# Kernel optimization log

Hardware: AMD Instinct MI355X
Metric: run time of the kernel (lower is better)

Reference implementation:

```python
import jax, jax.numpy as jnp
import numpy as np

B, S, E, H, M, Q = 2, 2048, 768, 12, 768, 4
D = E // H  # head_dim = 64
EPS = 1e-5


def _layernorm(x, g, b):
    m = jnp.mean(x, axis=-1, keepdims=True)
    v = jnp.mean((x - m) ** 2, axis=-1, keepdims=True)
    return (x - m) / jnp.sqrt(v + EPS) * g + b


def setup_inputs() -> dict:
    key = jax.random.key(0)
    ks = jax.random.split(key, 12)
    w = lambda k, shape, s=0.02: (jax.random.normal(k, shape) * s).astype(jnp.float32)
    return {
        "x": jax.random.normal(ks[0], (B, S, E), dtype=jnp.float32),
        "ln1_g": jnp.ones((E,), jnp.float32), "ln1_b": jnp.zeros((E,), jnp.float32),
        "wq": w(ks[1], (E, E)), "bq": jnp.zeros((E,), jnp.float32),
        "wk": w(ks[2], (E, E)), "bk": jnp.zeros((E,), jnp.float32),
        "wv": w(ks[3], (E, E)), "bv": jnp.zeros((E,), jnp.float32),
        "wo": w(ks[4], (E, E)), "bo": jnp.zeros((E,), jnp.float32),
        "ln2_g": jnp.ones((E,), jnp.float32), "ln2_b": jnp.zeros((E,), jnp.float32),
        "w1": w(ks[5], (E, Q * M)), "b1": jnp.zeros((Q * M,), jnp.float32),
        "wvqc": w(ks[6], (M, M)), "bvqc": jnp.zeros((M,), jnp.float32),
        "w2": w(ks[7], (Q * M, E)), "b2": jnp.zeros((E,), jnp.float32),
    }


def reference(x, ln1_g, ln1_b, wq, bq, wk, bk, wv, bv, wo, bo,
              ln2_g, ln2_b, w1, b1, wvqc, bvqc, w2, b2):
    b, s, e = x.shape
    h, d = H, e // H

    # --- attention branch (pre-norm, per-query-L2-normalized logits) ---
    xn = _layernorm(x, ln1_g, ln1_b)
    q = (xn @ wq + bq).reshape(b, s, h, d).transpose(0, 2, 1, 3)  # bhsd
    k = (xn @ wk + bk).reshape(b, s, h, d).transpose(0, 2, 1, 3)
    v = (xn @ wv + bv).reshape(b, s, h, d).transpose(0, 2, 1, 3)

    qk = jnp.einsum('bhsd,bhtd->bhst', q, k)                       # [B,H,S,S]
    q_norm2 = jnp.clip(jnp.sum(q * q, axis=-1, keepdims=True), 1e-5)  # [B,H,S,1]
    logits = qk / jnp.sqrt(d * q_norm2)
    attn = jax.nn.softmax(logits, axis=-1)
    vals = jnp.einsum('bhst,bhtd->bhsd', attn, v)
    vals = vals.transpose(0, 2, 1, 3).reshape(b, s, e)
    x = x + (vals @ wo + bo)  # residual; attn dropout is identity in eval

    # --- quantum-style FeedForward with overlapping q_stride slices ---
    xn2 = _layernorm(x, ln2_g, ln2_b)
    hmid = xn2 @ w1 + b1                                           # [B,S,Q*M]
    m = wvqc.shape[0]
    qstride = w1.shape[1] // m
    # overlapping slices h[..., i:i+M] for i in 0..Q-1, stacked on a new axis
    sl = jnp.stack([hmid[..., i:i + m] for i in range(qstride)], axis=2)  # [B,S,Q,M]
    hv = sl @ wvqc + bvqc                                          # vqc linear
    hv = hv.transpose(0, 1, 3, 2).reshape(b, s, qstride * m)       # interleave
    hv = jax.nn.gelu(hv, approximate=False)
    out = x + (hv @ w2 + b2)
    return out
```

## Files before the change

kernel.cpp:

```cpp
#include <hip/hip_runtime.h>
#include <hip/hip_bf16.h>
#include <math.h>

typedef unsigned short ushort_t;
typedef __attribute__((ext_vector_type(4))) short s16x4;
typedef __attribute__((ext_vector_type(8))) short short8;
typedef __attribute__((ext_vector_type(8))) __bf16 bf16x8;
typedef __attribute__((ext_vector_type(4))) float f32x4;
typedef __attribute__((ext_vector_type(4))) unsigned u32x4;

#define SDIM 2048
#define EDIM 768
#define NTOK 4096

static __device__ __forceinline__ ushort_t f2bf(float f) {
  unsigned u = __builtin_bit_cast(unsigned, f);
  u += 0x7fff + ((u >> 16) & 1);
  return (ushort_t)(u >> 16);
}
static __device__ __forceinline__ float bf2f(ushort_t h) {
  return __builtin_bit_cast(float, (unsigned)h << 16);
}
static __device__ __forceinline__ f32x4 mfma16(short8 a, short8 b, f32x4 c) {
  return __builtin_amdgcn_mfma_f32_16x16x32_bf16(
      __builtin_bit_cast(bf16x8, a), __builtin_bit_cast(bf16x8, b), c, 0, 0, 0);
}
static __device__ __forceinline__ void gload_lds16(const void* g, void* l) {
  __builtin_amdgcn_global_load_lds(
      (const __attribute__((address_space(1))) void*)g,
      (__attribute__((address_space(3))) void*)l, 16, 0, 0);
}
static __device__ __forceinline__ unsigned cvtpk(float lo, float hi) {
  unsigned r;
  asm("v_cvt_pk_bf16_f32 %0, %1, %2" : "=v"(r) : "v"(lo), "v"(hi));
  return r;
}
static __device__ __forceinline__ float exp2fast(float x) {
  float r;
  asm("v_exp_f32 %0, %1" : "=v"(r) : "v"(x));
  return r;
}

__global__ void k_pre(const float* __restrict__ wq, const float* __restrict__ wk,
                      const float* __restrict__ wv, const float* __restrict__ wo,
                      const float* __restrict__ wvqc, const float* __restrict__ w2,
                      const float* __restrict__ w1, const float* __restrict__ x,
                      const float* __restrict__ ln1g, const float* __restrict__ ln1b,
                      ushort_t* __restrict__ oqkv, ushort_t* __restrict__ owo,
                      ushort_t* __restrict__ ovqc, ushort_t* __restrict__ w2T,
                      ushort_t* __restrict__ w1s, ushort_t* __restrict__ xn) {
  const int y = blockIdx.y;
  const int tx = threadIdx.x, ty = threadIdx.y;
  __shared__ float tile[32][33];
  __shared__ float red[8];
  if (y < 216) {
    const float* in;
    ushort_t* out;
    int R, r0;
    const int c0 = blockIdx.x * 32;
    if (y < 120) {
      const int z = y / 24, ry = y - z * 24;
      in = z == 0 ? wq : z == 1 ? wk : z == 2 ? wv : z == 3 ? wo : wvqc;
      out = z < 3 ? oqkv + (size_t)z * 768 * 768 : (z == 3 ? owo : ovqc);
      R = 768;
      r0 = ry * 32;
    } else {
      in = w2;
      out = w2T;
      R = 3072;
      r0 = (y - 120) * 32;
    }
#pragma unroll
    for (int i = 0; i < 32; i += 8)
      tile[ty + i][tx] = in[(size_t)(r0 + ty + i) * 768 + c0 + tx];
    __syncthreads();
#pragma unroll
    for (int i = 0; i < 32; i += 8)
      out[(size_t)(c0 + ty + i) * R + r0 + tx] = f2bf(tile[tx][ty + i]);
  } else if (y < 312) {
    const int idx = ((y - 216) * 24 + blockIdx.x) * 256 + ty * 32 + tx;
    const int e = idx / 768, m = idx - (idx / 768) * 768;
#pragma unroll
    for (int i = 0; i < 4; i++)
      w1s[((size_t)i * 768 + e) * 768 + m] = f2bf(w1[(size_t)e * 3072 + i + m]);
  } else {
    const int row = (y - 312) * 24 + blockIdx.x;
    if (row >= NTOK) return;
    const int t = ty * 32 + tx;
    const float* xr = x + (size_t)row * EDIM;
    float v0 = xr[t], v1 = xr[t + 256], v2 = xr[t + 512];
    float s = v0 + v1 + v2;
    float s2 = v0 * v0 + v1 * v1 + v2 * v2;
#pragma unroll
    for (int m = 32; m; m >>= 1) {
      s += __shfl_xor(s, m);
      s2 += __shfl_xor(s2, m);
    }
    const int wid = t >> 6, lane = t & 63;
    if (lane == 0) { red[wid] = s; red[4 + wid] = s2; }
    __syncthreads();
    s = red[0] + red[1] + red[2] + red[3];
    s2 = red[4] + red[5] + red[6] + red[7];
    float mean = s * (1.f / EDIM);
    float var = s2 * (1.f / EDIM) - mean * mean;
    float rstd = rsqrtf(var + 1e-5f);
    ushort_t* orow = xn + (size_t)row * EDIM;
    orow[t] = f2bf((v0 - mean) * rstd * ln1g[t] + ln1b[t]);
    orow[t + 256] = f2bf((v1 - mean) * rstd * ln1g[t + 256] + ln1b[t + 256]);
    orow[t + 512] = f2bf((v2 - mean) * rstd * ln1g[t + 512] + ln1b[t + 512]);
  }
}

__global__ void k_vT(const ushort_t* __restrict__ in, ushort_t* __restrict__ out) {
  __shared__ ushort_t tile[32][34];
  int bh = blockIdx.z;
  int t0 = blockIdx.x * 32, d0 = blockIdx.y * 32;
  const ushort_t* ib = in + (size_t)bh * SDIM * 64;
  ushort_t* ob = out + (size_t)bh * 64 * SDIM;
  int tx = threadIdx.x, ty = threadIdx.y;
#pragma unroll
  for (int i = 0; i < 32; i += 8)
    tile[ty + i][tx] = ib[(size_t)(t0 + ty + i) * 64 + d0 + tx];
  __syncthreads();
  const int T = t0 + tx, tb = T & ~63, tl = T & 63;
  const int tperm =
      tb + 32 * (tl >> 5) + 8 * ((tl >> 2) & 3) + 4 * ((tl >> 4) & 1) + (tl & 3);
#pragma unroll
  for (int i = 0; i < 32; i += 8)
    ob[(size_t)(d0 + ty + i) * SDIM + tperm] = tile[tx][ty + i];
}

__global__ __launch_bounds__(256) void k_b1eff(const float* __restrict__ b1,
                                               const ushort_t* __restrict__ wvqcT,
                                               const float* __restrict__ bvqc,
                                               float* __restrict__ b1e) {
  const int n = blockIdx.x;
  const int i = n & 3, j = n >> 2;
  const int t = threadIdx.x;
  float s = 0.f;
  for (int m = t; m < 768; m += 256)
    s += b1[i + m] * bf2f(wvqcT[(size_t)j * 768 + m]);
#pragma unroll
  for (int mm = 32; mm; mm >>= 1) s += __shfl_xor(s, mm);
  __shared__ float red[4];
  if ((t & 63) == 0) red[t >> 6] = s;
  __syncthreads();
  if (t == 0) b1e[n] = red[0] + red[1] + red[2] + red[3] + bvqc[j];
}

__global__ __launch_bounds__(256) void k_ln(const float* __restrict__ x,
                                            const float* __restrict__ gam,
                                            const float* __restrict__ bet,
                                            ushort_t* __restrict__ out) {
  const int row = blockIdx.x, t = threadIdx.x;
  const float* xr = x + (size_t)row * EDIM;
  float v0 = xr[t], v1 = xr[t + 256], v2 = xr[t + 512];
  float s = v0 + v1 + v2;
  float s2 = v0 * v0 + v1 * v1 + v2 * v2;
#pragma unroll
  for (int m = 32; m; m >>= 1) { s += __shfl_xor(s, m); s2 += __shfl_xor(s2, m); }
  __shared__ float red[8];
  const int wid = t >> 6, lane = t & 63;
  if (lane == 0) { red[wid] = s; red[4 + wid] = s2; }
  __syncthreads();
  s = red[0] + red[1] + red[2] + red[3];
  s2 = red[4] + red[5] + red[6] + red[7];
  float mean = s * (1.f / EDIM);
  float var = s2 * (1.f / EDIM) - mean * mean;
  float rstd = rsqrtf(var + 1e-5f);
  ushort_t* orow = out + (size_t)row * EDIM;
  orow[t] = f2bf((v0 - mean) * rstd * gam[t] + bet[t]);
  orow[t + 256] = f2bf((v1 - mean) * rstd * gam[t + 256] + bet[t + 256]);
  orow[t + 512] = f2bf((v2 - mean) * rstd * gam[t + 512] + bet[t + 512]);
}

template <int MODE, int BM, int BN, int BK>
__global__ __launch_bounds__(256) void k_gemm(
    const ushort_t* __restrict__ A, const ushort_t* __restrict__ Bt, int lda,
    int ldb, int kc, const float* __restrict__ b0, const float* __restrict__ b1p,
    const float* __restrict__ b2p, float* __restrict__ outF,
    const float* __restrict__ resid, ushort_t* __restrict__ o0,
    ushort_t* __restrict__ o1, ushort_t* __restrict__ o2, int ldc) {
  constexpr int MT = BM / 32, NT = BN / 32;
  constexpr int KCH = BK / 8;
  constexpr int NPA = BM * BK / 2048;
  constexpr int NPB = BN * BK / 2048;
  constexpr int ROWSP = 2048 / BK;
  constexpr int KK = BK / 32;
  __shared__ ushort_t As[2][BM * BK];
  __shared__ ushort_t Bs[2][BN * BK];
  const int t = threadIdx.x;
  const int m0 = blockIdx.x * BM, n0 = blockIdx.y * BN;
  if (MODE == 3) Bt += (size_t)blockIdx.z * 768 * 768;
  const int koff = (MODE == 5) ? blockIdx.z * kc : 0;
  const int srow = t / KCH, sch = t % KCH;
  const int xs = (BK == 64) ? (srow & 7) : ((srow >> 1) & 3);
  const int gseg = (sch ^ xs) * 8;
  const ushort_t* ga = A + (size_t)(m0 + srow) * lda + koff + gseg;
  const ushort_t* gb = Bt + (size_t)(n0 + srow) * ldb + koff + gseg;
  const int ldst = t * 8;
  const int lane = t & 63, wid = t >> 6;
  const int g = lane >> 4, c = lane & 15;
  const int wm = (wid >> 1) * (BM / 2), wn = (wid & 1) * (BN / 2);
  const int xc = (BK == 64) ? (c & 7) : ((c >> 1) & 3);
  f32x4 acc[MT][NT] = {};

#define STAGE(BUF, K0)                                                           \
  {                                                                              \
    _Pragma("unroll") for (int p = 0; p < NPA; p++)                              \
        gload_lds16(ga + (K0) + (size_t)(p * ROWSP) * lda,                       \
                    As[BUF] + p * 2048 + ldst);                                  \
    _Pragma("unroll") for (int p = 0; p < NPB; p++)                              \
        gload_lds16(gb + (K0) + (size_t)(p * ROWSP) * ldb,                       \
                    Bs[BUF] + p * 2048 + ldst);                                  \
  }

  STAGE(0, 0);
  __syncthreads();
  int cur = 0;
  for (int k0 = 0; k0 < kc; k0 += BK) {
    if (k0 + BK < kc) STAGE(cur ^ 1, k0 + BK);
    short8 af[KK][MT], bfr[KK][NT];
#pragma unroll
    for (int kk = 0; kk < KK; kk++) {
#pragma unroll
      for (int mt = 0; mt < MT; mt++)
        af[kk][mt] = *(const short8*)(As[cur] + (wm + mt * 16 + c) * BK +
                                      (((g + kk * 4) ^ xc) * 8));
#pragma unroll
      for (int nt = 0; nt < NT; nt++)
        bfr[kk][nt] = *(const short8*)(Bs[cur] + (wn + nt * 16 + c) * BK +
                                       (((g + kk * 4) ^ xc) * 8));
    }
    __builtin_amdgcn_s_setprio(1);
#pragma unroll
    for (int kk = 0; kk < KK; kk++)
#pragma unroll
      for (int mt = 0; mt < MT; mt++)
#pragma unroll
        for (int nt = 0; nt < NT; nt++)
          acc[mt][nt] = mfma16(af[kk][mt], bfr[kk][nt], acc[mt][nt]);
    __builtin_amdgcn_s_setprio(0);
    __syncthreads();
    cur ^= 1;
  }
#undef STAGE

#pragma unroll
  for (int mt = 0; mt < MT; mt++) {
#pragma unroll
    for (int nt = 0; nt < NT; nt++) {
#pragma unroll
      for (int r = 0; r < 4; r++) {
        int row = m0 + wm + mt * 16 + g * 4 + r;
        int col = n0 + wn + nt * 16 + c;
        float val = acc[mt][nt][r];
        if constexpr (MODE == 0) {
          int which = col / 768;
          int nn = col - which * 768;
          int h = nn >> 6, d = nn & 63;
          int bb = row >> 11, s = row & 2047;
          const float* bp = which == 0 ? b0 : (which == 1 ? b1p : b2p);
          ushort_t* dp = which == 0 ? o0 : (which == 1 ? o1 : o2);
          dp[(((size_t)(bb * 12 + h)) * SDIM + s) * 64 + d] = f2bf(val + bp[nn]);
        } else if constexpr (MODE == 1) {
          size_t o = (size_t)row * ldc + col;
          outF[o] = resid[o] + val + b0[col];
        } else if constexpr (MODE == 2) {
          float xg = val + b0[col];
          float z2 = xg * (1.5957691216f + 0.0713548162f * xg * xg);
          float ge = xg / (1.f + __expf(-z2));
          o0[(size_t)row * ldc + col] = f2bf(ge);
        } else if constexpr (MODE == 5) {
          o0[(size_t)blockIdx.z * (NTOK * 768) + (size_t)row * ldc + col] =
              f2bf(val);
        } else {
          o0[((size_t)row * 4 + blockIdx.z) * ldc + col] = f2bf(val);
        }
      }
    }
  }
}

__global__ __launch_bounds__(256) void k_attn(
    const ushort_t* __restrict__ q, const ushort_t* __restrict__ k,
    const ushort_t* __restrict__ vt, ushort_t* __restrict__ o0p,
    ushort_t* __restrict__ o1p, float* __restrict__ lpart) {
  const int tid = threadIdx.x;
  const int wid = tid >> 6, lane = tid & 63;
  const int g = lane >> 4, c = lane & 15;
  const int bh = blockIdx.y;
  const int z = blockIdx.z;
  const int tbase = z * (SDIM / 2);
  const int q0 = blockIdx.x * 128 + wid * 32;
  const int bb = bh / 12, h = bh - bb * 12;
  const ushort_t* qb = q + (size_t)bh * SDIM * 64;
  const ushort_t* kb = k + (size_t)bh * SDIM * 64;
  const ushort_t* vb = vt + (size_t)bh * 64 * SDIM;

  __shared__ ushort_t Ks[2][64 * 64];
  __shared__ ushort_t Vs[2][64 * 64];

  short8 bq[2][2];
#pragma unroll
  for (int qg = 0; qg < 2; qg++) {
    short8 a0 = *(const short8*)(qb + (size_t)(q0 + qg * 16 + c) * 64 + g * 8);
    short8 a1 =
        *(const short8*)(qb + (size_t)(q0 + qg * 16 + c) * 64 + 32 + g * 8);
    float s = 0.f;
#pragma unroll
    for (int j = 0; j < 8; j++) {
      float f0 = bf2f((ushort_t)a0[j]), f1 = bf2f((ushort_t)a1[j]);
      s += f0 * f0 + f1 * f1;
    }
    s += __shfl_xor(s, 16);
    s += __shfl_xor(s, 32);
    const float scq = rsqrtf(64.f * fmaxf(s, 1e-5f)) * 1.44269504089f;
#pragma unroll
    for (int j = 0; j < 8; j++) {
      bq[qg][0][j] = (short)f2bf(bf2f((ushort_t)a0[j]) * scq);
      bq[qg][1][j] = (short)f2bf(bf2f((ushort_t)a1[j]) * scq);
    }
  }
  const short8 ones = {0x3F80, 0x3F80, 0x3F80, 0x3F80,
                       0x3F80, 0x3F80, 0x3F80, 0x3F80};

  const int srow = tid >> 3, sj = tid & 7;

#define STAGE(BUF, T0)                                                          \
  {                                                                             \
    _Pragma("unroll") for (int n = 0; n < 2; n++) {                             \
      const int row = n * 32 + srow;                                            \
      const int scol = (sj ^ (row & 7)) * 8;                                    \
      gload_lds16(kb + (size_t)((T0) + row) * 64 + scol,                        \
                  Ks[BUF] + n * 2048 + tid * 8);                                \
      gload_lds16(vb + (size_t)row * SDIM + (T0) + scol,                        \
                  Vs[BUF] + n * 2048 + tid * 8);                                \
    }                                                                           \
  }

  f32x4 accO[2][4] = {};
  f32x4 accL[2] = {};
  const int sw = (c & 7) << 4;

  STAGE(0, tbase);
  __syncthreads();
  int cur = 0;
  for (int tt = 0; tt < SDIM / 128; tt++) {
    const int t0 = tbase + tt * 64;
    if (tt + 1 < SDIM / 128) STAGE(cur ^ 1, t0 + 64);
    const char* Kc = (const char*)Ks[cur];
    const char* Vc = (const char*)Vs[cur];
    f32x4 s0[4] = {}, s1[4] = {};
    __builtin_amdgcn_s_setprio(1);
#pragma unroll
    for (int i = 0; i < 4; i++) {
      const int rb = (i * 16 + c) * 128;
      short8 ka0 = *(const short8*)(Kc + rb + ((g * 16) ^ sw));
      short8 ka1 = *(const short8*)(Kc + rb + ((64 + g * 16) ^ sw));
      s0[i] = mfma16(ka0, bq[0][0], s0[i]);
      s1[i] = mfma16(ka0, bq[1][0], s1[i]);
      s0[i] = mfma16(ka1, bq[0][1], s0[i]);
      s1[i] = mfma16(ka1, bq[1][1], s1[i]);
    }
    __builtin_amdgcn_s_setprio(0);
    u32x4 w00 = {cvtpk(exp2fast(s0[0][0]), exp2fast(s0[0][1])),
                 cvtpk(exp2fast(s0[0][2]), exp2fast(s0[0][3])),
                 cvtpk(exp2fast(s0[1][0]), exp2fast(s0[1][1])),
                 cvtpk(exp2fast(s0[1][2]), exp2fast(s0[1][3]))};
    u32x4 w10 = {cvtpk(exp2fast(s1[0][0]), exp2fast(s1[0][1])),
                 cvtpk(exp2fast(s1[0][2]), exp2fast(s1[0][3])),
                 cvtpk(exp2fast(s1[1][0]), exp2fast(s1[1][1])),
                 cvtpk(exp2fast(s1[1][2]), exp2fast(s1[1][3]))};
    u32x4 w01 = {cvtpk(exp2fast(s0[2][0]), exp2fast(s0[2][1])),
                 cvtpk(exp2fast(s0[2][2]), exp2fast(s0[2][3])),
                 cvtpk(exp2fast(s0[3][0]), exp2fast(s0[3][1])),
                 cvtpk(exp2fast(s0[3][2]), exp2fast(s0[3][3]))};
    u32x4 w11 = {cvtpk(exp2fast(s1[2][0]), exp2fast(s1[2][1])),
                 cvtpk(exp2fast(s1[2][2]), exp2fast(s1[2][3])),
                 cvtpk(exp2fast(s1[3][0]), exp2fast(s1[3][1])),
                 cvtpk(exp2fast(s1[3][2]), exp2fast(s1[3][3]))};
    short8 pa00 = __builtin_bit_cast(short8, w00);
    short8 pa01 = __builtin_bit_cast(short8, w01);
    short8 pa10 = __builtin_bit_cast(short8, w10);
    short8 pa11 = __builtin_bit_cast(short8, w11);
    __builtin_amdgcn_s_setprio(1);
    accL[0] = mfma16(pa00, ones, accL[0]);
    accL[1] = mfma16(pa10, ones, accL[1]);
    accL[0] = mfma16(pa01, ones, accL[0]);
    accL[1] = mfma16(pa11, ones, accL[1]);
#pragma unroll
    for (int dt = 0; dt < 4; dt++) {
      const int vbse = (dt * 16 + c) * 128;
      short8 v0 = *(const short8*)(Vc + vbse + ((g * 16) ^ sw));
      short8 v1 = *(const short8*)(Vc + vbse + ((64 + g * 16) ^ sw));
      accO[0][dt] = mfma16(pa00, v0, accO[0][dt]);
      accO[1][dt] = mfma16(pa10, v0, accO[1][dt]);
      accO[0][dt] = mfma16(pa01, v1, accO[0][dt]);
      accO[1][dt] = mfma16(pa11, v1, accO[1][dt]);
    }
    __builtin_amdgcn_s_setprio(0);
    __syncthreads();
    cur ^= 1;
  }
#undef STAGE

  ushort_t* op = z ? o1p : o0p;
#pragma unroll
  for (int qg = 0; qg < 2; qg++) {
    if (c == 0) {
#pragma unroll
      for (int r = 0; r < 4; r++)
        lpart[((size_t)z * 24 + bh) * SDIM + q0 + qg * 16 + 4 * g + r] =
            accL[qg][r];
    }
#pragma unroll
    for (int dt = 0; dt < 4; dt++)
#pragma unroll
      for (int r = 0; r < 4; r++) {
        int s = q0 + qg * 16 + 4 * g + r;
        op[((size_t)(bb * SDIM + s)) * EDIM + h * 64 + dt * 16 + c] =
            f2bf(accO[qg][dt][r]);
      }
  }
}

__global__ __launch_bounds__(256) void k_comb(const ushort_t* __restrict__ o0p,
                                              const ushort_t* __restrict__ o1p,
                                              const float* __restrict__ lpart,
                                              ushort_t* __restrict__ vals) {
  const int gid = blockIdx.x * 256 + threadIdx.x;
  const int tok = gid / 96, ch = gid - tok * 96;
  const int h = ch >> 3;
  const int bb = tok >> 11, s = tok & 2047;
  const size_t lrow = (size_t)(bb * 12 + h) * SDIM + s;
  const float inv = 1.f / (lpart[lrow] + lpart[(size_t)24 * SDIM + lrow]);
  short8 a = *(const short8*)(o0p + (size_t)gid * 8);
  short8 b = *(const short8*)(o1p + (size_t)gid * 8);
  short8 o;
#pragma unroll
  for (int j = 0; j < 8; j++)
    o[j] = (short)f2bf((bf2f((ushort_t)a[j]) + bf2f((ushort_t)b[j])) * inv);
  *(short8*)(vals + (size_t)gid * 8) = o;
}

__global__ __launch_bounds__(256) void k_fin(const float* __restrict__ x2,
                                             const float* __restrict__ b2,
                                             const ushort_t* __restrict__ p,
                                             float* __restrict__ out) {
  const int i = blockIdx.x * 256 + threadIdx.x;
  f32x4 r = ((const f32x4*)x2)[i];
  f32x4 b = ((const f32x4*)b2)[i % 192];
  s16x4 a0 = ((const s16x4*)p)[i];
  s16x4 a1 = ((const s16x4*)(p + (size_t)NTOK * 768))[i];
  f32x4 o;
#pragma unroll
  for (int j = 0; j < 4; j++)
    o[j] = r[j] + b[j] + bf2f((ushort_t)a0[j]) + bf2f((ushort_t)a1[j]);
  ((f32x4*)out)[i] = o;
}

extern "C" void kernel_launch(void* const* d_in, const int* in_sizes, int n_in,
                              void* d_out, int out_size, void* d_ws, size_t ws_size,
                              hipStream_t stream) {
  const float* x = (const float*)d_in[0];
  const float* ln1g = (const float*)d_in[1];
  const float* ln1b = (const float*)d_in[2];
  const float* wq = (const float*)d_in[3];
  const float* bq = (const float*)d_in[4];
  const float* wk = (const float*)d_in[5];
  const float* bk = (const float*)d_in[6];
  const float* wv = (const float*)d_in[7];
  const float* bv = (const float*)d_in[8];
  const float* wo = (const float*)d_in[9];
  const float* bo = (const float*)d_in[10];
  const float* ln2g = (const float*)d_in[11];
  const float* ln2b = (const float*)d_in[12];
  const float* w1 = (const float*)d_in[13];
  const float* b1 = (const float*)d_in[14];
  const float* wvqc = (const float*)d_in[15];
  const float* bvqc = (const float*)d_in[16];
  const float* w2 = (const float*)d_in[17];
  const float* b2 = (const float*)d_in[18];
  float* out = (float*)d_out;

  char* w = (char*)d_ws;
  ushort_t* xn = (ushort_t*)(w + 0);
  ushort_t* vtb = (ushort_t*)(w + 0);
  ushort_t* xn2 = (ushort_t*)(w + 6291456);
  ushort_t* opart1 = (ushort_t*)(w + 6291456);
  float* x2 = (float*)(w + 12582912);
  ushort_t* qb = (ushort_t*)(w + 25165824);
  ushort_t* kb = (ushort_t*)(w + 31457280);
  ushort_t* vb = (ushort_t*)(w + 37748736);
  ushort_t* vals = (ushort_t*)(w + 44040192);
  ushort_t* G = (ushort_t*)(w + 25165824);
  ushort_t* wqkvT = (ushort_t*)(w + 50528256);
  ushort_t* woT = (ushort_t*)(w + 54067200);
  ushort_t* wvqcT = (ushort_t*)(w + 55246848);
  ushort_t* w1s = (ushort_t*)(w + 56426496);
  float* lpart = (float*)(w + 56426496);
  ushort_t* W1eT = (ushort_t*)(w + 61145088);
  float* b1e = (float*)(w + 65863680);
  ushort_t* w2T = (ushort_t*)(w + 65875968);
  ushort_t* mp = (ushort_t*)(w + 0);

  dim3 tb(32, 8);
  k_pre<<<dim3(24, 483), tb, 0, stream>>>(wq, wk, wv, wo, wvqc, w2, w1, x, ln1g,
                                          ln1b, wqkvT, woT, wvqcT, w2T, w1s, xn);
  k_b1eff<<<3072, 256, 0, stream>>>(b1, wvqcT, bvqc, b1e);
  k_gemm<3, 64, 64, 64><<<dim3(12, 12, 4), 256, 0, stream>>>(
      wvqcT, w1s, 768, 768, 768, nullptr, nullptr, nullptr, nullptr, nullptr,
      W1eT, nullptr, nullptr, 768);
  k_gemm<0, 128, 64, 64><<<dim3(32, 36), 256, 0, stream>>>(
      xn, wqkvT, 768, 768, 768, bq, bk, bv, nullptr, nullptr, qb, kb, vb, 0);
  k_vT<<<dim3(64, 2, 24), tb, 0, stream>>>(vb, vtb);
  k_attn<<<dim3(16, 24, 2), 256, 0, stream>>>(qb, kb, vtb, vals, opart1, lpart);
  k_comb<<<1536, 256, 0, stream>>>(vals, opart1, lpart, vals);
  k_gemm<1, 64, 64, 64><<<dim3(64, 12), 256, 0, stream>>>(
      vals, woT, 768, 768, 768, bo, nullptr, nullptr, x2, x, nullptr, nullptr,
      nullptr, 768);
  k_ln<<<4096, 256, 0, stream>>>(x2, ln2g, ln2b, xn2);
  k_gemm<2, 128, 64, 64><<<dim3(32, 48), 256, 0, stream>>>(
      xn2, W1eT, 768, 768, 768, b1e, nullptr, nullptr, nullptr, nullptr, G,
      nullptr, nullptr, 3072);
  k_gemm<5, 64, 64, 64><<<dim3(64, 12, 2), 256, 0, stream>>>(
      G, w2T, 3072, 3072, 1536, nullptr, nullptr, nullptr, nullptr, nullptr, mp,
      nullptr, nullptr, 768);
  k_fin<<<3072, 256, 0, stream>>>(x2, b2, mp, out);
}
```

Before: 192.8 us.

## Fold bias precompute into prep kernel, widen attention tiles, drop split-K FFN2

The separate b1-effective kernel becomes an extra block row of the prep kernel, computed serially per thread from fp32 wvqc. The attention kernel now gives each wave 64 queries instead of 32, which halves the grid and reuses each K/V LDS tile across more queries. The final FFN GEMM drops split-K plus the separate finish kernel and uses the fused bias+residual epilogue (mode 1) over the full K=3072. This removes launches and an intermediate round trip. In exchange it raises register pressure in attention, lowers grid parallelism, and makes the folded bias loop slow and serial.

New measurement: 232.7 us. +20.7%, slower.

```diff
diff --git a/kernel.cpp b/kernel.cpp
--- a/kernel.cpp
+++ b/kernel.cpp
@@ -3,7 +3,6 @@
 #include <math.h>
 
 typedef unsigned short ushort_t;
-typedef __attribute__((ext_vector_type(4))) short s16x4;
 typedef __attribute__((ext_vector_type(8))) short short8;
 typedef __attribute__((ext_vector_type(8))) __bf16 bf16x8;
 typedef __attribute__((ext_vector_type(4))) float f32x4;
@@ -46,9 +45,11 @@
                       const float* __restrict__ wvqc, const float* __restrict__ w2,
                       const float* __restrict__ w1, const float* __restrict__ x,
                       const float* __restrict__ ln1g, const float* __restrict__ ln1b,
+                      const float* __restrict__ b1, const float* __restrict__ bvqc,
                       ushort_t* __restrict__ oqkv, ushort_t* __restrict__ owo,
                       ushort_t* __restrict__ ovqc, ushort_t* __restrict__ w2T,
-                      ushort_t* __restrict__ w1s, ushort_t* __restrict__ xn) {
+                      ushort_t* __restrict__ w1s, ushort_t* __restrict__ xn,
+                      float* __restrict__ b1e) {
   const int y = blockIdx.y;
   const int tx = threadIdx.x, ty = threadIdx.y;
   __shared__ float tile[32][33];
@@ -83,7 +84,7 @@
 #pragma unroll
     for (int i = 0; i < 4; i++)
       w1s[((size_t)i * 768 + e) * 768 + m] = f2bf(w1[(size_t)e * 3072 + i + m]);
-  } else {
+  } else if (y < 483) {
     const int row = (y - 312) * 24 + blockIdx.x;
     if (row >= NTOK) return;
     const int t = ty * 32 + tx;
@@ -108,6 +109,13 @@
     orow[t] = f2bf((v0 - mean) * rstd * ln1g[t] + ln1b[t]);
     orow[t + 256] = f2bf((v1 - mean) * rstd * ln1g[t + 256] + ln1b[t + 256]);
     orow[t + 512] = f2bf((v2 - mean) * rstd * ln1g[t + 512] + ln1b[t + 512]);
+  } else {
+    const int n = blockIdx.x * 256 + ty * 32 + tx;
+    if (n >= 3072) return;
+    const int i = n & 3, j = n >> 2;
+    float s = 0.f;
+    for (int m = 0; m < 768; m++) s += b1[i + m] * wvqc[(size_t)m * 768 + j];
+    b1e[n] = s + bvqc[j];
   }
 }
 
@@ -128,24 +136,6 @@
 #pragma unroll
   for (int i = 0; i < 32; i += 8)
     ob[(size_t)(d0 + ty + i) * SDIM + tperm] = tile[tx][ty + i];
-}
-
-__global__ __launch_bounds__(256) void k_b1eff(const float* __restrict__ b1,
-                                               const ushort_t* __restrict__ wvqcT,
-                                               const float* __restrict__ bvqc,
-                                               float* __restrict__ b1e) {
-  const int n = blockIdx.x;
-  const int i = n & 3, j = n >> 2;
-  const int t = threadIdx.x;
-  float s = 0.f;
-  for (int m = t; m < 768; m += 256)
-    s += b1[i + m] * bf2f(wvqcT[(size_t)j * 768 + m]);
-#pragma unroll
-  for (int mm = 32; mm; mm >>= 1) s += __shfl_xor(s, mm);
-  __shared__ float red[4];
-  if ((t & 63) == 0) red[t >> 6] = s;
-  __syncthreads();
-  if (t == 0) b1e[n] = red[0] + red[1] + red[2] + red[3] + bvqc[j];
 }
 
 __global__ __launch_bounds__(256) void k_ln(const float* __restrict__ x,
@@ -192,12 +182,11 @@
   const int t = threadIdx.x;
   const int m0 = blockIdx.x * BM, n0 = blockIdx.y * BN;
   if (MODE == 3) Bt += (size_t)blockIdx.z * 768 * 768;
-  const int koff = (MODE == 5) ? blockIdx.z * kc : 0;
   const int srow = t / KCH, sch = t % KCH;
   const int xs = (BK == 64) ? (srow & 7) : ((srow >> 1) & 3);
   const int gseg = (sch ^ xs) * 8;
-  const ushort_t* ga = A + (size_t)(m0 + srow) * lda + koff + gseg;
-  const ushort_t* gb = Bt + (size_t)(n0 + srow) * ldb + koff + gseg;
+  const ushort_t* ga = A + (size_t)(m0 + srow) * lda + gseg;
+  const ushort_t* gb = Bt + (size_t)(n0 + srow) * ldb + gseg;
   const int ldst = t * 8;
   const int lane = t & 63, wid = t >> 6;
   const int g = lane >> 4, c = lane & 15;
@@ -271,9 +260,6 @@
           float z2 = xg * (1.5957691216f + 0.0713548162f * xg * xg);
           float ge = xg / (1.f + __expf(-z2));
           o0[(size_t)row * ldc + col] = f2bf(ge);
-        } else if constexpr (MODE == 5) {
-          o0[(size_t)blockIdx.z * (NTOK * 768) + (size_t)row * ldc + col] =
-              f2bf(val);
         } else {
           o0[((size_t)row * 4 + blockIdx.z) * ldc + col] = f2bf(val);
         }
@@ -292,7 +278,7 @@
   const int bh = blockIdx.y;
   const int z = blockIdx.z;
   const int tbase = z * (SDIM / 2);
-  const int q0 = blockIdx.x * 128 + wid * 32;
+  const int q0 = blockIdx.x * 256 + wid * 64;
   const int bb = bh / 12, h = bh - bb * 12;
   const ushort_t* qb = q + (size_t)bh * SDIM * 64;
   const ushort_t* kb = k + (size_t)bh * SDIM * 64;
@@ -301,9 +287,9 @@
   __shared__ ushort_t Ks[2][64 * 64];
   __shared__ ushort_t Vs[2][64 * 64];
 
-  short8 bq[2][2];
-#pragma unroll
-  for (int qg = 0; qg < 2; qg++) {
+  short8 bq[4][2];
+#pragma unroll
+  for (int qg = 0; qg < 4; qg++) {
     short8 a0 = *(const short8*)(qb + (size_t)(q0 + qg * 16 + c) * 64 + g * 8);
     short8 a1 =
         *(const short8*)(qb + (size_t)(q0 + qg * 16 + c) * 64 + 32 + g * 8);
@@ -339,8 +325,8 @@
     }                                                                           \
   }
 
-  f32x4 accO[2][4] = {};
-  f32x4 accL[2] = {};
+  f32x4 accO[4][4] = {};
+  f32x4 accL[4] = {};
   const int sw = (c & 7) << 4;
 
   STAGE(0, tbase);
@@ -351,55 +337,60 @@
     if (tt + 1 < SDIM / 128) STAGE(cur ^ 1, t0 + 64);
     const char* Kc = (const char*)Ks[cur];
     const char* Vc = (const char*)Vs[cur];
-    f32x4 s0[4] = {}, s1[4] = {};
+    f32x4 s[4][4] = {};
     __builtin_amdgcn_s_setprio(1);
 #pragma unroll
     for (int i = 0; i < 4; i++) {
       const int rb = (i * 16 + c) * 128;
       short8 ka0 = *(const short8*)(Kc + rb + ((g * 16) ^ sw));
       short8 ka1 = *(const short8*)(Kc + rb + ((64 + g * 16) ^ sw));
-      s0[i] = mfma16(ka0, bq[0][0], s0[i]);
-      s1[i] = mfma16(ka0, bq[1][0], s1[i]);
-      s0[i] = mfma16(ka1, bq[0][1], s0[i]);
-      s1[i] = mfma16(ka1, bq[1][1], s1[i]);
+#pragma unroll
+      for (int qg = 0; qg < 4; qg++) {
+        s[qg][i] = mfma16(ka0, bq[qg][0], s[qg][i]);
+        s[qg][i] = mfma16(ka1, bq[qg][1], s[qg][i]);
+      }
     }
     __builtin_amdgcn_s_setprio(0);
-    u32x4 w00 = {cvtpk(exp2fast(s0[0][0]), exp2fast(s0[0][1])),
-                 cvtpk(exp2fast(s0[0][2]), exp2fast(s0[0][3])),
-                 cvtpk(exp2fast(s0[1][0]), exp2fast(s0[1][1])),
-                 cvtpk(exp2fast(s0[1][2]), exp2fast(s0[1][3]))};
-    u32x4 w10 = {cvtpk(exp2fast(s1[0][0]), exp2fast(s1[0][1])),
-                 cvtpk(exp2fast(s1[0][2]), exp2fast(s1[0][3])),
-                 cvtpk(exp2fast(s1[1][0]), exp2fast(s1[1][1])),
-                 cvtpk(exp2fast(s1[1][2]), exp2fast(s1[1][3]))};
-    u32x4 w01 = {cvtpk(exp2fast(s0[2][0]), exp2fast(s0[2][1])),
-                 cvtpk(exp2fast(s0[2][2]), exp2fast(s0[2][3])),
-                 cvtpk(exp2fast(s0[3][0]), exp2fast(s0[3][1])),
-                 cvtpk(exp2fast(s0[3][2]), exp2fast(s0[3][3]))};
-    u32x4 w11 = {cvtpk(exp2fast(s1[2][0]), exp2fast(s1[2][1])),
-                 cvtpk(exp2fast(s1[2][2]), exp2fast(s1[2][3])),
-                 cvtpk(exp2fast(s1[3][0]), exp2fast(s1[3][1])),
-                 cvtpk(exp2fast(s1[3][2]), exp2fast(s1[3][3]))};
-    short8 pa00 = __builtin_bit_cast(short8, w00);
-    short8 pa01 = __builtin_bit_cast(short8, w01);
-    short8 pa10 = __builtin_bit_cast(short8, w10);
-    short8 pa11 = __builtin_bit_cast(short8, w11);
-    __builtin_amdgcn_s_setprio(1);
-    accL[0] = mfma16(pa00, ones, accL[0]);
-    accL[1] = mfma16(pa10, ones, accL[1]);
-    accL[0] = mfma16(pa01, ones, accL[0]);
-    accL[1] = mfma16(pa11, ones, accL[1]);
-#pragma unroll
-    for (int dt = 0; dt < 4; dt++) {
-      const int vbse = (dt * 16 + c) * 128;
-      short8 v0 = *(const short8*)(Vc + vbse + ((g * 16) ^ sw));
-      short8 v1 = *(const short8*)(Vc + vbse + ((64 + g * 16) ^ sw));
-      accO[0][dt] = mfma16(pa00, v0, accO[0][dt]);
-      accO[1][dt] = mfma16(pa10, v0, accO[1][dt]);
-      accO[0][dt] = mfma16(pa01, v1, accO[0][dt]);
-      accO[1][dt] = mfma16(pa11, v1, accO[1][dt]);
-    }
-    __builtin_amdgcn_s_setprio(0);
+#pragma unroll
+    for (int pr = 0; pr < 2; pr++) {
+      const int ca = pr * 2, cbx = pr * 2 + 1;
+      u32x4 wa0 = {cvtpk(exp2fast(s[ca][0][0]), exp2fast(s[ca][0][1])),
+                   cvtpk(exp2fast(s[ca][0][2]), exp2fast(s[ca][0][3])),
+                   cvtpk(exp2fast(s[ca][1][0]), exp2fast(s[ca][1][1])),
+                   cvtpk(exp2fast(s[ca][1][2]), exp2fast(s[ca][1][3]))};
+      u32x4 wb0 = {cvtpk(exp2fast(s[cbx][0][0]), exp2fast(s[cbx][0][1])),
+                   cvtpk(exp2fast(s[cbx][0][2]), exp2fast(s[cbx][0][3])),
+                   cvtpk(exp2fast(s[cbx][1][0]), exp2fast(s[cbx][1][1])),
+                   cvtpk(exp2fast(s[cbx][1][2]), exp2fast(s[cbx][1][3]))};
+      u32x4 wa1 = {cvtpk(exp2fast(s[ca][2][0]), exp2fast(s[ca][2][1])),
+                   cvtpk(exp2fast(s[ca][2][2]), exp2fast(s[ca][2][3])),
+                   cvtpk(exp2fast(s[ca][3][0]), exp2fast(s[ca][3][1])),
+                   cvtpk(exp2fast(s[ca][3][2]), exp2fast(s[ca][3][3]))};
+      u32x4 wb1 = {cvtpk(exp2fast(s[cbx][2][0]), exp2fast(s[cbx][2][1])),
+                   cvtpk(exp2fast(s[cbx][2][2]), exp2fast(s[cbx][2][3])),
+                   cvtpk(exp2fast(s[cbx][3][0]), exp2fast(s[cbx][3][1])),
+                   cvtpk(exp2fast(s[cbx][3][2]), exp2fast(s[cbx][3][3]))};
+      short8 paa0 = __builtin_bit_cast(short8, wa0);
+      short8 paa1 = __builtin_bit_cast(short8, wa1);
+      short8 pab0 = __builtin_bit_cast(short8, wb0);
+      short8 pab1 = __builtin_bit_cast(short8, wb1);
+      __builtin_amdgcn_s_setprio(1);
+      accL[ca] = mfma16(paa0, ones, accL[ca]);
+      accL[cbx] = mfma16(pab0, ones, accL[cbx]);
+      accL[ca] = mfma16(paa1, ones, accL[ca]);
+      accL[cbx] = mfma16(pab1, ones, accL[cbx]);
+#pragma unroll
+      for (int dt = 0; dt < 4; dt++) {
+        const int vbse = (dt * 16 + c) * 128;
+        short8 v0 = *(const short8*)(Vc + vbse + ((g * 16) ^ sw));
+        short8 v1 = *(const short8*)(Vc + vbse + ((64 + g * 16) ^ sw));
+        accO[ca][dt] = mfma16(paa0, v0, accO[ca][dt]);
+        accO[cbx][dt] = mfma16(pab0, v0, accO[cbx][dt]);
+        accO[ca][dt] = mfma16(paa1, v1, accO[ca][dt]);
+        accO[cbx][dt] = mfma16(pab1, v1, accO[cbx][dt]);
+      }
+      __builtin_amdgcn_s_setprio(0);
+    }
     __syncthreads();
     cur ^= 1;
   }
@@ -407,7 +398,7 @@
 
   ushort_t* op = z ? o1p : o0p;
 #pragma unroll
-  for (int qg = 0; qg < 2; qg++) {
+  for (int qg = 0; qg < 4; qg++) {
     if (c == 0) {
 #pragma unroll
       for (int r = 0; r < 4; r++)
@@ -442,22 +433,6 @@
   for (int j = 0; j < 8; j++)
     o[j] = (short)f2bf((bf2f((ushort_t)a[j]) + bf2f((ushort_t)b[j])) * inv);
   *(short8*)(vals + (size_t)gid * 8) = o;
-}
-
-__global__ __launch_bounds__(256) void k_fin(const float* __restrict__ x2,
-                                             const float* __restrict__ b2,
-                                             const ushort_t* __restrict__ p,
-                                             float* __restrict__ out) {
-  const int i = blockIdx.x * 256 + threadIdx.x;
-  f32x4 r = ((const f32x4*)x2)[i];
-  f32x4 b = ((const f32x4*)b2)[i % 192];
-  s16x4 a0 = ((const s16x4*)p)[i];
-  s16x4 a1 = ((const s16x4*)(p + (size_t)NTOK * 768))[i];
-  f32x4 o;
-#pragma unroll
-  for (int j = 0; j < 4; j++)
-    o[j] = r[j] + b[j] + bf2f((ushort_t)a0[j]) + bf2f((ushort_t)a1[j]);
-  ((f32x4*)out)[i] = o;
 }
 
 extern "C" void kernel_launch(void* const* d_in, const int* in_sizes, int n_in,
@@ -503,19 +478,18 @@
   ushort_t* W1eT = (ushort_t*)(w + 61145088);
   float* b1e = (float*)(w + 65863680);
   ushort_t* w2T = (ushort_t*)(w + 65875968);
-  ushort_t* mp = (ushort_t*)(w + 0);
 
   dim3 tb(32, 8);
-  k_pre<<<dim3(24, 483), tb, 0, stream>>>(wq, wk, wv, wo, wvqc, w2, w1, x, ln1g,
-                                          ln1b, wqkvT, woT, wvqcT, w2T, w1s, xn);
-  k_b1eff<<<3072, 256, 0, stream>>>(b1, wvqcT, bvqc, b1e);
+  k_pre<<<dim3(24, 484), tb, 0, stream>>>(wq, wk, wv, wo, wvqc, w2, w1, x, ln1g,
+                                          ln1b, b1, bvqc, wqkvT, woT, wvqcT, w2T,
+                                          w1s, xn, b1e);
   k_gemm<3, 64, 64, 64><<<dim3(12, 12, 4), 256, 0, stream>>>(
       wvqcT, w1s, 768, 768, 768, nullptr, nullptr, nullptr, nullptr, nullptr,
       W1eT, nullptr, nullptr, 768);
   k_gemm<0, 128, 64, 64><<<dim3(32, 36), 256, 0, stream>>>(
       xn, wqkvT, 768, 768, 768, bq, bk, bv, nullptr, nullptr, qb, kb, vb, 0);
   k_vT<<<dim3(64, 2, 24), tb, 0, stream>>>(vb, vtb);
-  k_attn<<<dim3(16, 24, 2), 256, 0, stream>>>(qb, kb, vtb, vals, opart1, lpart);
+  k_attn<<<dim3(8, 24, 2), 256, 0, stream>>>(qb, kb, vtb, vals, opart1, lpart);
   k_comb<<<1536, 256, 0, stream>>>(vals, opart1, lpart, vals);
   k_gemm<1, 64, 64, 64><<<dim3(64, 12), 256, 0, stream>>>(
       vals, woT, 768, 768, 768, bo, nullptr, nullptr, x2, x, nullptr, nullptr,
@@ -524,8 +498,7 @@
   k_gemm<2, 128, 64, 64><<<dim3(32, 48), 256, 0, stream>>>(
       xn2, W1eT, 768, 768, 768, b1e, nullptr, nullptr, nullptr, nullptr, G,
       nullptr, nullptr, 3072);
-  k_gemm<5, 64, 64, 64><<<dim3(64, 12, 2), 256, 0, stream>>>(
-      G, w2T, 3072, 3072, 1536, nullptr, nullptr, nullptr, nullptr, nullptr, mp,
-      nullptr, nullptr, 768);
-  k_fin<<<3072, 256, 0, stream>>>(x2, b2, mp, out);
-}
+  k_gemm<1, 64, 64, 64><<<dim3(64, 12), 256, 0, stream>>>(
+      G, w2T, 3072, 3072, 3072, b2, nullptr, nullptr, out, x2, nullptr, nullptr,
+      nullptr, 768);
+}
```
